# Performance work log

Measured on AMD Instinct MI355X. Metric: run time of the kernel, lower is better.

## Reference

```python
import jax, jax.numpy as jnp
import numpy as np


def setup_inputs() -> dict:
    key = jax.random.key(0)
    k1, k2 = jax.random.split(key)
    B, C, T = 32, 64, 16384
    x = jax.random.normal(k1, (B, C, T), dtype=jnp.float32)
    # learned scalar threshold parameter (init 0.1 in the torch module)
    threshold = jnp.asarray(0.1, dtype=jnp.float32)
    return {"x": x, "threshold": threshold}


def reference(x, threshold):
    """Delta-modulation encoder: x (B,C,T) -> spikes (B,C,T) in {-1,0,1}."""
    th = jnp.clip(threshold, 0.01, 0.5)

    def step(recon, xt):
        # recon, xt: (B, C)
        err = xt - recon
        pos = (err > th).astype(xt.dtype)
        neg = (err < -th).astype(xt.dtype)
        net = pos - neg
        recon = recon + net * th
        return recon, net

    x_t = jnp.moveaxis(x, 2, 0)  # (T, B, C): scan over time
    recon0 = jnp.zeros_like(x[:, :, 0])
    _, spikes = jax.lax.scan(step, recon0, x_t)
    return jnp.moveaxis(spikes, 0, 2)  # back to (B, C, T)
```

## Files before the change

kernel.cpp:

```cpp
#include <hip/hip_runtime.h>
#include <stdint.h>


constexpr int T_LEN  = 16384;
constexpr int W      = 512;
constexpr int NWIN   = T_LEN / W;
constexpr int K      = 8;
constexpr int HALF_G = K * W / 4;

typedef __attribute__((address_space(3))) uint32_t lds_u32;
typedef __attribute__((address_space(1))) uint32_t glb_u32;

__device__ __forceinline__ void gld_lds16(const float* gsrc, float4* ldst) {
    __builtin_amdgcn_global_load_lds((const glb_u32*)gsrc, (lds_u32*)ldst, 16, 0, 0);
}

__device__ __forceinline__ void stage_window(const float* __restrict__ x,
                                             int seq_base, int nseq, int win,
                                             float4* lds_half, int lane) {
    const int c  = lane >> 3;
    const int m4 = (lane & 7) ^ c;
    int seq = seq_base + c;
    if (seq >= nseq) seq = nseq - 1;
    const float* src0 = x + (size_t)seq * T_LEN + (size_t)win * W + m4 * 4;
    #pragma unroll
    for (int k = 0; k < W / 32; ++k) {
        gld_lds16(src0 + k * 32, lds_half + k * 64);
    }
}

__device__ __forceinline__ float dm_step(const float xv, float& r, const float th) {
    const float err = xv - r;
    const bool  m   = fabsf(err) > th;
    const float rc  = r + copysignf(th, err);
    const float o   = m ? copysignf(1.0f, err) : 0.0f;
    r = m ? rc : r;
    return o;
}

__device__ __forceinline__ float4 step4(const float4 xv, float& r, const float th) {
    float4 o;
    o.x = dm_step(xv.x, r, th);
    o.y = dm_step(xv.y, r, th);
    o.z = dm_step(xv.z, r, th);
    o.w = dm_step(xv.w, r, th);
    return o;
}

#define LOADG(d, g)                                                     \
    d##0 = lb[(g) * 64 + (0 ^ c)]; d##1 = lb[(g) * 64 + (1 ^ c)];       \
    d##2 = lb[(g) * 64 + (2 ^ c)]; d##3 = lb[(g) * 64 + (3 ^ c)];       \
    d##4 = lb[(g) * 64 + (4 ^ c)]; d##5 = lb[(g) * 64 + (5 ^ c)];       \
    d##6 = lb[(g) * 64 + (6 ^ c)]; d##7 = lb[(g) * 64 + (7 ^ c)];

#define COMPG(s, g)                                                     \
    pw[(g) * 8 + 0] = step4(s##0, r, th);                               \
    pw[(g) * 8 + 1] = step4(s##1, r, th);                               \
    pw[(g) * 8 + 2] = step4(s##2, r, th);                               \
    pw[(g) * 8 + 3] = step4(s##3, r, th);                               \
    pw[(g) * 8 + 4] = step4(s##4, r, th);                               \
    pw[(g) * 8 + 5] = step4(s##5, r, th);                               \
    pw[(g) * 8 + 6] = step4(s##6, r, th);                               \
    pw[(g) * 8 + 7] = step4(s##7, r, th);

__global__ void __launch_bounds__(64, 1)
dm_encode_kernel(const float* __restrict__ x,
                 const float* __restrict__ thp,
                 float* __restrict__ out,
                 const int nseq) {
    __shared__ float4 xb4[2 * HALF_G];

    const int lane     = threadIdx.x;
    const int seq_base = blockIdx.x * K;
    const float th     = fminf(fmaxf(thp[0], 0.01f), 0.5f);

    stage_window(x, seq_base, nseq, 0, xb4, lane);

    const int  c    = lane;
    const bool comp = (lane < K) && (seq_base + lane < nseq);
    float r = 0.0f;
    float4* po = nullptr;
    if (comp) po = reinterpret_cast<float4*>(out + (size_t)(seq_base + c) * T_LEN);

    for (int win = 0; win < NWIN; ++win) {
        const int half = win & 1;

        asm volatile("s_waitcnt vmcnt(0)" ::: "memory");

        if (win + 1 < NWIN)
            stage_window(x, seq_base, nseq, win + 1,
                         xb4 + (half ^ 1) * HALF_G, lane);

        if (comp) {
            const float4* lb = xb4 + half * HALF_G + c * 8;
            float4* pw = po + win * (W / 4);

            float4 a0, a1, a2, a3, a4, a5, a6, a7;
            float4 b0, b1, b2, b3, b4, b5, b6, b7;
            LOADG(a, 0)

            #pragma unroll 1
            for (int i = 0; i < 7; ++i) {
                const int gA = 2 * i;
                LOADG(b, gA + 1)
                COMPG(a, gA)
                LOADG(a, gA + 2)
                COMPG(b, gA + 1)
            }
            LOADG(b, 15)
            COMPG(a, 14)
            COMPG(b, 15)
        }
    }
}

extern "C" void kernel_launch(void* const* d_in, const int* in_sizes, int n_in,
                              void* d_out, int out_size, void* d_ws, size_t ws_size,
                              hipStream_t stream) {
    const float* x   = (const float*)d_in[0];
    const float* thp = (const float*)d_in[1];
    float* out       = (float*)d_out;

    const int nseq = in_sizes[0] / T_LEN;
    const int grid = (nseq + K - 1) / K;

    dm_encode_kernel<<<grid, 64, 0, stream>>>(x, thp, out, nseq);
}
```

Before: 529.4 us.

## Deepen LDS prefetch to four groups, relax vmcnt wait, add fast step path

Reorganizes the per-window inner loop to keep four float4 groups in flight instead of two, giving the LDS reads more time to land before the serial recurrence consumes them. The global-to-LDS wait is relaxed from vmcnt(0) to vmcnt(48) after the first window, so output stores no longer stall the next window's staging. It also adds a templated fast path that computes the spike as d*inv, with one fewer select on the serial chain, and picks it when th*inv rounds exactly to 1. This costs more registers and code size, and the relaxed wait depends on how the store and load counts are ordered.

```diff
diff --git a/kernel.cpp b/kernel.cpp
--- a/kernel.cpp
+++ b/kernel.cpp
@@ -18,62 +18,63 @@
 __device__ __forceinline__ void stage_window(const float* __restrict__ x,
                                              int seq_base, int nseq, int win,
                                              float4* lds_half, int lane) {
-    const int c  = lane >> 3;
-    const int m4 = (lane & 7) ^ c;
-    int seq = seq_base + c;
+    const int cc = lane >> 3;
+    const int m4 = (lane & 7) ^ cc;
+    int seq = seq_base + cc;
     if (seq >= nseq) seq = nseq - 1;
     const float* src0 = x + (size_t)seq * T_LEN + (size_t)win * W + m4 * 4;
     #pragma unroll
-    for (int k = 0; k < W / 32; ++k) {
+    for (int k = 0; k < W / 32; ++k)
         gld_lds16(src0 + k * 32, lds_half + k * 64);
-    }
 }
 
-__device__ __forceinline__ float dm_step(const float xv, float& r, const float th) {
+template<bool FAST>
+__device__ __forceinline__ float dm_step(const float xv, float& r,
+                                         const float th, const float inv) {
     const float err = xv - r;
-    const bool  m   = fabsf(err) > th;
-    const float rc  = r + copysignf(th, err);
-    const float o   = m ? copysignf(1.0f, err) : 0.0f;
-    r = m ? rc : r;
+    const float s   = __builtin_copysignf(th, err);
+    const bool  m   = __builtin_fabsf(err) > th;
+    const float d   = m ? s : 0.0f;
+    r += d;
+    if (FAST) return d * inv;
+    const float t = __builtin_copysignf(1.0f, err);
+    return m ? t : 0.0f;
+}
+
+template<bool FAST>
+__device__ __forceinline__ float4 step4(const float4 xv, float& r,
+                                        const float th, const float inv) {
+    float4 o;
+    o.x = dm_step<FAST>(xv.x, r, th, inv);
+    o.y = dm_step<FAST>(xv.y, r, th, inv);
+    o.z = dm_step<FAST>(xv.z, r, th, inv);
+    o.w = dm_step<FAST>(xv.w, r, th, inv);
     return o;
 }
 
-__device__ __forceinline__ float4 step4(const float4 xv, float& r, const float th) {
-    float4 o;
-    o.x = dm_step(xv.x, r, th);
-    o.y = dm_step(xv.y, r, th);
-    o.z = dm_step(xv.z, r, th);
-    o.w = dm_step(xv.w, r, th);
-    return o;
-}
+#define LOADG(P, g)                                                       \
+    P##0 = lb[(g) * 64 + (0 ^ c)]; P##1 = lb[(g) * 64 + (1 ^ c)];         \
+    P##2 = lb[(g) * 64 + (2 ^ c)]; P##3 = lb[(g) * 64 + (3 ^ c)];         \
+    P##4 = lb[(g) * 64 + (4 ^ c)]; P##5 = lb[(g) * 64 + (5 ^ c)];         \
+    P##6 = lb[(g) * 64 + (6 ^ c)]; P##7 = lb[(g) * 64 + (7 ^ c)];
 
-#define LOADG(d, g)                                                     \
-    d##0 = lb[(g) * 64 + (0 ^ c)]; d##1 = lb[(g) * 64 + (1 ^ c)];       \
-    d##2 = lb[(g) * 64 + (2 ^ c)]; d##3 = lb[(g) * 64 + (3 ^ c)];       \
-    d##4 = lb[(g) * 64 + (4 ^ c)]; d##5 = lb[(g) * 64 + (5 ^ c)];       \
-    d##6 = lb[(g) * 64 + (6 ^ c)]; d##7 = lb[(g) * 64 + (7 ^ c)];
+#define COMPG(P, g)                                                       \
+    pw[(g) * 8 + 0] = step4<FAST>(P##0, r, th, inv);                      \
+    pw[(g) * 8 + 1] = step4<FAST>(P##1, r, th, inv);                      \
+    pw[(g) * 8 + 2] = step4<FAST>(P##2, r, th, inv);                      \
+    pw[(g) * 8 + 3] = step4<FAST>(P##3, r, th, inv);                      \
+    pw[(g) * 8 + 4] = step4<FAST>(P##4, r, th, inv);                      \
+    pw[(g) * 8 + 5] = step4<FAST>(P##5, r, th, inv);                      \
+    pw[(g) * 8 + 6] = step4<FAST>(P##6, r, th, inv);                      \
+    pw[(g) * 8 + 7] = step4<FAST>(P##7, r, th, inv);
 
-#define COMPG(s, g)                                                     \
-    pw[(g) * 8 + 0] = step4(s##0, r, th);                               \
-    pw[(g) * 8 + 1] = step4(s##1, r, th);                               \
-    pw[(g) * 8 + 2] = step4(s##2, r, th);                               \
-    pw[(g) * 8 + 3] = step4(s##3, r, th);                               \
-    pw[(g) * 8 + 4] = step4(s##4, r, th);                               \
-    pw[(g) * 8 + 5] = step4(s##5, r, th);                               \
-    pw[(g) * 8 + 6] = step4(s##6, r, th);                               \
-    pw[(g) * 8 + 7] = step4(s##7, r, th);
-
-__global__ void __launch_bounds__(64, 1)
-dm_encode_kernel(const float* __restrict__ x,
-                 const float* __restrict__ thp,
-                 float* __restrict__ out,
-                 const int nseq) {
-    __shared__ float4 xb4[2 * HALF_G];
-
-    const int lane     = threadIdx.x;
-    const int seq_base = blockIdx.x * K;
-    const float th     = fminf(fmaxf(thp[0], 0.01f), 0.5f);
-
+template<bool FAST>
+__device__ __forceinline__ void run(float4* __restrict__ xb4,
+                                    const float* __restrict__ x,
+                                    float* __restrict__ out,
+                                    const float th, const float inv,
+                                    const int seq_base, const int nseq,
+                                    const int lane) {
     stage_window(x, seq_base, nseq, 0, xb4, lane);
 
     const int  c    = lane;
@@ -85,7 +86,8 @@
     for (int win = 0; win < NWIN; ++win) {
         const int half = win & 1;
 
-        asm volatile("s_waitcnt vmcnt(0)" ::: "memory");
+        if (win == 0) asm volatile("s_waitcnt vmcnt(0)" ::: "memory");
+        else          asm volatile("s_waitcnt vmcnt(48)" ::: "memory");
 
         if (win + 1 < NWIN)
             stage_window(x, seq_base, nseq, win + 1,
@@ -95,23 +97,45 @@
             const float4* lb = xb4 + half * HALF_G + c * 8;
             float4* pw = po + win * (W / 4);
 
-            float4 a0, a1, a2, a3, a4, a5, a6, a7;
-            float4 b0, b1, b2, b3, b4, b5, b6, b7;
-            LOADG(a, 0)
+            float4 A0, A1, A2, A3, A4, A5, A6, A7;
+            float4 B0, B1, B2, B3, B4, B5, B6, B7;
+            float4 C0, C1, C2, C3, C4, C5, C6, C7;
+            float4 D0, D1, D2, D3, D4, D5, D6, D7;
 
+            LOADG(A, 0)
+            LOADG(B, 1)
             #pragma unroll 1
-            for (int i = 0; i < 7; ++i) {
-                const int gA = 2 * i;
-                LOADG(b, gA + 1)
-                COMPG(a, gA)
-                LOADG(a, gA + 2)
-                COMPG(b, gA + 1)
+            for (int k2 = 0; k2 < 3; ++k2) {
+                const int g = 4 * k2;
+                LOADG(C, g + 2) COMPG(A, g)
+                LOADG(D, g + 3) COMPG(B, g + 1)
+                LOADG(A, g + 4) COMPG(C, g + 2)
+                LOADG(B, g + 5) COMPG(D, g + 3)
             }
-            LOADG(b, 15)
-            COMPG(a, 14)
-            COMPG(b, 15)
+            LOADG(C, 14) COMPG(A, 12)
+            LOADG(D, 15) COMPG(B, 13)
+            COMPG(C, 14)
+            COMPG(D, 15)
         }
     }
+}
+
+__global__ void __launch_bounds__(64, 1)
+dm_encode_kernel(const float* __restrict__ x,
+                 const float* __restrict__ thp,
+                 float* __restrict__ out,
+                 const int nseq) {
+    __shared__ float4 xb4[2 * HALF_G];
+
+    const int lane     = threadIdx.x;
+    const int seq_base = blockIdx.x * K;
+
+    const float th  = fminf(fmaxf(thp[0], 0.01f), 0.5f);
+    const float inv = 1.0f / th;
+    const bool fast = (th * inv == 1.0f);
+
+    if (fast) run<true >(xb4, x, out, th, inv, seq_base, nseq, lane);
+    else      run<false>(xb4, x, out, th, inv, seq_base, nseq, lane);
 }
 
 extern "C" void kernel_launch(void* const* d_in, const int* in_sizes, int n_in,
```

Measured after the change: 474.4 us. 1.12x faster.
